# Performance work log

Hardware: AMD Instinct MI355X
Metric: run time of the kernel (lower is better)

## Reference

```python
import jax, jax.numpy as jnp
import numpy as np

B, A, C = 16, 16384, 81
TOP_K = 50
CONF_THRESH = 0.5
IOU_THRESH = 0.5
VAR0, VAR1 = 0.1, 0.2          # cfg['variance']
IMG_HW = 1.0                   # cfg['min_dim']/img_size = 320/320
MIN_SIZE = 0.0
NEG = -jnp.inf


def setup_inputs() -> dict:
    key = jax.random.key(0)
    k1, k2, k3 = jax.random.split(key, 3)
    conf_preds = jax.random.uniform(k1, (B, A, C), dtype=jnp.float32)
    loc_delta = jax.random.normal(k2, (B, A, 4), dtype=jnp.float32)
    anchors = jax.random.uniform(k3, (A, 4), dtype=jnp.float32)  # cxcywh priors in [0,1)
    return {"conf_preds": conf_preds, "loc_delta": loc_delta, "anchors": anchors}


def _decode_clip(loc, anchors):
    # SSD decode: cxcy = prior_cxcy + loc_xy*v0*prior_wh ; wh = prior_wh*exp(loc_wh*v1)
    cxcy = anchors[..., :2] + loc[..., :2] * VAR0 * anchors[..., 2:]
    wh = anchors[..., 2:] * jnp.exp(loc[..., 2:] * VAR1)
    x1y1 = cxcy - wh * 0.5
    x2y2 = x1y1 + wh
    boxes = jnp.concatenate([x1y1, x2y2], axis=-1)  # [..., 4] xyxy
    return jnp.clip(boxes, 0.0, IMG_HW)            # clip_boxes_to_image((1,1))


def _nms_single(boxes, s):
    # boxes: [A,4] xyxy, s: [A] scores with invalid entries already at -inf.
    # Greedy NMS, fixed TOP_K iterations (torchvision semantics: suppress iou > thresh).
    areas = (boxes[:, 2] - boxes[:, 0]) * (boxes[:, 3] - boxes[:, 1])

    def step(s, _):
        i = jnp.argmax(s)
        take = s[i] > NEG
        b = boxes[i]
        xx1 = jnp.maximum(b[0], boxes[:, 0])
        yy1 = jnp.maximum(b[1], boxes[:, 1])
        xx2 = jnp.minimum(b[2], boxes[:, 2])
        yy2 = jnp.minimum(b[3], boxes[:, 3])
        inter = jnp.maximum(xx2 - xx1, 0.0) * jnp.maximum(yy2 - yy1, 0.0)
        iou = inter / (areas[i] + areas - inter)
        s = jnp.where(take & (iou > IOU_THRESH), NEG, s)
        s = s.at[i].set(NEG)  # guarantee progress
        return s, (i, take)

    _, (idx, take) = jax.lax.scan(step, s, None, length=TOP_K)
    return idx, take  # [TOP_K] int, [TOP_K] bool


def reference(conf_preds, loc_delta, anchors):
    boxes = _decode_clip(loc_delta, anchors)                # [B,A,4]
    conf = jnp.transpose(conf_preds, (0, 2, 1))             # [B,C,A]
    # remove_small_boxes(min_size=0) as a mask (all-true here, kept for fidelity)
    w = boxes[..., 2] - boxes[..., 0]
    h = boxes[..., 3] - boxes[..., 1]
    valid = (w >= MIN_SIZE) & (h >= MIN_SIZE)               # [B,A]
    masked = jnp.where((conf > CONF_THRESH) & valid[:, None, :], conf, NEG)  # [B,C,A]

    sg = jax.lax.stop_gradient
    nms_c = jax.vmap(_nms_single, in_axes=(None, 0))        # over classes
    nms_bc = jax.vmap(nms_c, in_axes=(0, 0))                # over batch
    idx, take = nms_bc(sg(boxes), sg(masked))               # [B,C,K]

    scores_sel = jnp.take_along_axis(conf, idx, axis=2)     # [B,C,K]
    b_idx = jnp.arange(boxes.shape[0])[:, None, None]
    boxes_sel = boxes[b_idx, idx]                           # [B,C,K,4]
    preds = jnp.concatenate([
        jnp.where(take, scores_sel, 0.0)[..., None],
        jnp.where(take[..., None], boxes_sel, 0.0),
    ], axis=-1)                                             # [B,C,K,5]
    return preds
```

## Files before the change

### kernel.cpp

```cpp
#include <hip/hip_runtime.h>
#include <math.h>

#define NB 16
#define NA 16384
#define NC 81
#define TOPK 50
#define TRC 4096
#define NEGF (-__builtin_inff())
#define SUPC 0.5000000298023223876953125

typedef unsigned long long ull;

#define WS_CONFT_OFF  ((size_t)4194304)
#define WS_FULL  (WS_CONFT_OFF + (size_t)NB * NC * NA * 2)

__global__ __launch_bounds__(256) void decode_k(const float* __restrict__ loc,
                                                const float* __restrict__ anc,
                                                float* __restrict__ boxes) {
#pragma clang fp contract(off)
    int i = blockIdx.x * 256 + threadIdx.x;
    if (i >= NB * NA) return;
    int a = i & (NA - 1);
    float4 an = ((const float4*)anc)[a];
    float4 ld = ((const float4*)loc)[i];
    float cx = an.x + (ld.x * 0.1f) * an.z;
    float cy = an.y + (ld.y * 0.1f) * an.w;
    float w = an.z * (float)exp((double)(ld.z * 0.2f));
    float h = an.w * (float)exp((double)(ld.w * 0.2f));
    float x1 = cx - w * 0.5f;
    float y1 = cy - h * 0.5f;
    float x2 = x1 + w;
    float y2 = y1 + h;
    x1 = fminf(fmaxf(x1, 0.f), 1.f);
    y1 = fminf(fmaxf(y1, 0.f), 1.f);
    x2 = fminf(fmaxf(x2, 0.f), 1.f);
    y2 = fminf(fmaxf(y2, 0.f), 1.f);
    ((float4*)boxes)[i] = make_float4(x1, y1, x2, y2);
}

__device__ __forceinline__ unsigned short enc_code(float v) {
    unsigned short e = 0xFFFFu;
    if (v > 0.5f) e = (unsigned short)(511u - ((__float_as_uint(v) >> 14) & 0x1FFu));
    return e;
}

#define TSLAB 256
__global__ __launch_bounds__(256) void transq_k(const float* __restrict__ conf,
                                                unsigned short* __restrict__ confT) {
    __shared__ unsigned short code[TSLAB * NC];
    const int b = blockIdx.y;
    const int slab = blockIdx.x;
    const float4* src = (const float4*)(conf + ((size_t)b * NA + (size_t)slab * TSLAB) * NC);
    const int t = threadIdx.x;
    for (int i = t; i < (TSLAB * NC) / 4; i += 256) {
        float4 v = src[i];
        unsigned f = 4u * (unsigned)i;
        unsigned a = f / (unsigned)NC;
        unsigned c = f - a * (unsigned)NC;
        code[c * TSLAB + a] = enc_code(v.x);
        if (++c == NC) { c = 0; ++a; }
        code[c * TSLAB + a] = enc_code(v.y);
        if (++c == NC) { c = 0; ++a; }
        code[c * TSLAB + a] = enc_code(v.z);
        if (++c == NC) { c = 0; ++a; }
        code[c * TSLAB + a] = enc_code(v.w);
    }
    __syncthreads();
    const int lane = t & 63, wv = t >> 6;
    for (int c = wv; c < NC; c += 4) {
        ull v = *(const ull*)&code[c * TSLAB + lane * 4];
        *(ull*)(confT + ((size_t)b * NC + c) * NA + (size_t)slab * TSLAB + lane * 4) = v;
    }
}

__global__ __launch_bounds__(256, 8) void nmsB4_k(const unsigned short* __restrict__ confT,
                                                  const float* __restrict__ conf,
                                                  const float* __restrict__ boxes,
                                                  float* __restrict__ out) {
#pragma clang fp contract(off)
    const int blk = blockIdx.x;
    const int b = blk / NC, c = blk - b * NC;
    const int t = threadIdx.x;
    const int lane = t & 63, wv = t >> 6;

    __shared__ unsigned short s_ix[TRC];
    __shared__ unsigned s_off[513];
    __shared__ unsigned s_aux[512];
    __shared__ float s_acc[TOPK][5];
    __shared__ float4 s_cbox[256];
    __shared__ unsigned long long s_kill[4];
    __shared__ int s_ctrl[16];

    const uint4* row8 = (const uint4*)(confT + ((size_t)b * NC + c) * NA);
    const float* cp = conf + ((size_t)b * NA) * NC + c;
    const float4* bb = (const float4*)boxes + (size_t)b * NA;
    float* orow = out + ((size_t)b * NC + c) * (TOPK * 5);

    for (int i = t; i < 512; i += 256) s_aux[i] = 0u;
    if (t == 0) { s_ctrl[0] = 0; s_ctrl[8] = 0; s_ctrl[12] = 0; }
    __syncthreads();
#pragma unroll
    for (int r = 0; r < 8; ++r) {
        uint4 q = row8[t + 256 * r];
        unsigned w;
        w = q.x; if ((w & 0xFFFFu) != 0xFFFFu) atomicAdd(&s_aux[w & 0xFFFFu], 1u);
                 if ((w >> 16)     != 0xFFFFu) atomicAdd(&s_aux[w >> 16], 1u);
        w = q.y; if ((w & 0xFFFFu) != 0xFFFFu) atomicAdd(&s_aux[w & 0xFFFFu], 1u);
                 if ((w >> 16)     != 0xFFFFu) atomicAdd(&s_aux[w >> 16], 1u);
        w = q.z; if ((w & 0xFFFFu) != 0xFFFFu) atomicAdd(&s_aux[w & 0xFFFFu], 1u);
                 if ((w >> 16)     != 0xFFFFu) atomicAdd(&s_aux[w >> 16], 1u);
        w = q.w; if ((w & 0xFFFFu) != 0xFFFFu) atomicAdd(&s_aux[w & 0xFFFFu], 1u);
                 if ((w >> 16)     != 0xFFFFu) atomicAdd(&s_aux[w >> 16], 1u);
    }
    __syncthreads();
    for (int i = t; i < 512; i += 256) atomicMax(&s_ctrl[8], (int)s_aux[i]);
    if (t == 0) s_off[0] = 0u;
    for (int i = t; i < 512; i += 256) s_off[i + 1] = s_aux[i];
    __syncthreads();
    for (int d = 1; d < 512; d <<= 1) {
        int i0 = 1 + t, i1 = 257 + t;
        unsigned v0 = (i0 - d >= 1) ? s_off[i0 - d] : 0u;
        unsigned v1 = (i1 - d >= 1) ? s_off[i1 - d] : 0u;
        __syncthreads();
        s_off[i0] += v0;
        s_off[i1] += v1;
        __syncthreads();
    }

    if (s_ctrl[8] <= TRC) {
        while (true) {
            if (t == 0) {
                int lo = s_ctrl[12];
                int hi = lo;
                while (hi < 512 && s_off[hi + 1] - s_off[lo] <= (unsigned)TRC) hi++;
                s_ctrl[13] = hi;
            }
            __syncthreads();
            const int trLo = s_ctrl[12], trHi = s_ctrl[13];
            const unsigned tbase = s_off[trLo], tend = s_off[trHi];
            if (tbase == tend) break;
            for (int i = trLo + t; i < trHi; i += 256) s_aux[i] = s_off[i] - tbase;
            __syncthreads();
#pragma unroll
            for (int r = 0; r < 8; ++r) {
                uint4 q = row8[t + 256 * r];
                int a0i = 8 * (t + 256 * r);
                unsigned w; int bk;
                w = q.x;
                bk = (int)(w & 0xFFFFu); if (bk >= trLo && bk < trHi) s_ix[atomicAdd(&s_aux[bk], 1u)] = (unsigned short)(a0i + 0);
                bk = (int)(w >> 16);     if (bk >= trLo && bk < trHi) s_ix[atomicAdd(&s_aux[bk], 1u)] = (unsigned short)(a0i + 1);
                w = q.y;
                bk = (int)(w & 0xFFFFu); if (bk >= trLo && bk < trHi) s_ix[atomicAdd(&s_aux[bk], 1u)] = (unsigned short)(a0i + 2);
                bk = (int)(w >> 16);     if (bk >= trLo && bk < trHi) s_ix[atomicAdd(&s_aux[bk], 1u)] = (unsigned short)(a0i + 3);
                w = q.z;
                bk = (int)(w & 0xFFFFu); if (bk >= trLo && bk < trHi) s_ix[atomicAdd(&s_aux[bk], 1u)] = (unsigned short)(a0i + 4);
                bk = (int)(w >> 16);     if (bk >= trLo && bk < trHi) s_ix[atomicAdd(&s_aux[bk], 1u)] = (unsigned short)(a0i + 5);
                w = q.w;
                bk = (int)(w & 0xFFFFu); if (bk >= trLo && bk < trHi) s_ix[atomicAdd(&s_aux[bk], 1u)] = (unsigned short)(a0i + 6);
                bk = (int)(w >> 16);     if (bk >= trLo && bk < trHi) s_ix[atomicAdd(&s_aux[bk], 1u)] = (unsigned short)(a0i + 7);
            }
            if (t == 0) s_ctrl[7] = trLo;
            __syncthreads();

            while (true) {
                if (t == 0) {
                    int bp = s_ctrl[7];
                    int mode;
                    if (bp >= trHi || s_off[bp] >= tend) {
                        mode = 2;
                    } else {
                        unsigned pos = s_off[bp] - tbase;
                        int bpl = bp;
                        unsigned q = pos;
                        for (int w = 0; w < 4; ++w) {
                            s_ctrl[2 + w] = (int)q;
                            while (bpl < trHi && (s_off[bpl + 1] - tbase - q) <= 64u) bpl++;
                            q = (bpl < trHi) ? s_off[bpl] - tbase : tend - tbase;
                        }
                        s_ctrl[6] = (int)q;
                        s_ctrl[7] = bpl;
                        mode = 0;
                        if (q == pos) {
                            mode = 1;
                            s_ctrl[9] = (int)pos;
                            s_ctrl[10] = (int)(s_off[bp + 1] - tbase);
                            s_ctrl[7] = bp + 1;
                        }
                    }
                    s_ctrl[11] = mode;
                }
                __syncthreads();
                const int mode = s_ctrl[11];
                if (mode == 2) break;
                const int nacc0 = s_ctrl[0];

                if (mode == 0) {
                    const unsigned q0 = (unsigned)s_ctrl[2 + wv];
                    const unsigned q1 = (unsigned)s_ctrl[3 + wv];
                    const int mw = (int)(q1 - q0);
                    const bool valid = lane < mw;
                    int ii = (int)q0 + lane; if (ii > TRC - 1) ii = TRC - 1;
                    int a = valid ? (int)s_ix[ii] : 0;
                    float4 bxv = bb[a];
                    if (!valid) bxv = make_float4(0.f, 0.f, 0.f, 0.f);
                    s_cbox[wv * 64 + lane] = bxv;
                    float mar = (bxv.z - bxv.x) * (bxv.w - bxv.y);
                    bool kill = !valid;
                    for (int j = 0; j < nacc0; ++j) {
                        float xx1 = fmaxf(s_acc[j][0], bxv.x), yy1 = fmaxf(s_acc[j][1], bxv.y);
                        float xx2 = fminf(s_acc[j][2], bxv.z), yy2 = fminf(s_acc[j][3], bxv.w);
                        float iw = fmaxf(xx2 - xx1, 0.f), ih = fmaxf(yy2 - yy1, 0.f);
                        float inter = iw * ih;
                        float den = (s_acc[j][4] + mar) - inter;
                        if ((double)inter > (double)den * SUPC) kill = true;
                    }
                    unsigned long long km = __ballot(kill);
                    if (lane == 0) s_kill[wv] = km;
                    __syncthreads();

                    if (wv == 0) {
                        int na = nacc0;
                        for (int cc = 0; cc < 4 && na < TOPK; ++cc) {
                            const unsigned e0 = (unsigned)s_ctrl[2 + cc];
                            const unsigned e1 = (unsigned)s_ctrl[3 + cc];
                            const int mc = (int)(e1 - e0);
                            if (mc <= 0) continue;
                            unsigned long long alive = ~s_kill[cc];
                            if (mc < 64) alive &= (1ull << mc) - 1ull;
                            int jj = (int)e0 + lane; if (jj > TRC - 1) jj = TRC - 1;
                            int aj = (lane < mc) ? (int)s_ix[jj] : 0;
                            float myscore = cp[(size_t)aj * NC];
                            float4 mybx = s_cbox[cc * 64 + lane];
                            float mar2 = (mybx.z - mybx.x) * (mybx.w - mybx.y);
                            for (int j = nacc0; j < na && alive; ++j) {
                                float xx1 = fmaxf(s_acc[j][0], mybx.x), yy1 = fmaxf(s_acc[j][1], mybx.y);
                                float xx2 = fminf(s_acc[j][2], mybx.z), yy2 = fminf(s_acc[j][3], mybx.w);
                                float iw = fmaxf(xx2 - xx1, 0.f), ih = fmaxf(yy2 - yy1, 0.f);
                                float inter = iw * ih;
                                float den = (s_acc[j][4] + mar2) - inter;
                                bool sup = ((double)inter > (double)den * SUPC);
                                alive &= ~__ballot(sup);
                            }
                            unsigned long long mykey =
                                ((unsigned long long)__float_as_uint(myscore) << 32) |
                                (unsigned)(16383 - aj);
                            while (alive && na < TOPK) {
                                unsigned long long kk = ((alive >> lane) & 1ull) ? mykey : 0ull;
                                int src = lane;
                                for (int off = 32; off; off >>= 1) {
                                    unsigned long long ok = __shfl_xor(kk, off);
                                    int osrc = __shfl_xor(src, off);
                                    if (ok > kk) { kk = ok; src = osrc; }
                                }
                                float4 wb = s_cbox[cc * 64 + src];
                                float wscore = __shfl(myscore, src);
                                float war = (wb.z - wb.x) * (wb.w - wb.y);
                                if (lane == 0) {
                                    orow[na * 5 + 0] = wscore;
                                    orow[na * 5 + 1] = wb.x; orow[na * 5 + 2] = wb.y;
                                    orow[na * 5 + 3] = wb.z; orow[na * 5 + 4] = wb.w;
                                    s_acc[na][0] = wb.x; s_acc[na][1] = wb.y;
                                    s_acc[na][2] = wb.z; s_acc[na][3] = wb.w;
                                    s_acc[na][4] = war;
                                }
                                na++;
                                alive &= ~(1ull << src);
                                if (alive) {
                                    float xx1 = fmaxf(wb.x, mybx.x), yy1 = fmaxf(wb.y, mybx.y);
                                    float xx2 = fminf(wb.z, mybx.z), yy2 = fminf(wb.w, mybx.w);
                                    float iw = fmaxf(xx2 - xx1, 0.f), ih = fmaxf(yy2 - yy1, 0.f);
                                    float inter = iw * ih;
                                    float den = (war + mar2) - inter;
                                    bool sup = ((double)inter > (double)den * SUPC);
                                    alive &= ~__ballot(sup);
                                }
                            }
                        }
                        if (lane == 0) s_ctrl[0] = na;
                    }
                    __syncthreads();
                } else {
                    const int e0 = s_ctrl[9], e1 = s_ctrl[10];
                    if (wv == 0) {
                        int na = s_ctrl[0];
                        while (na < TOPK) {
                            unsigned long long bk = 0ull; int bpos = 0;
                            for (int i = e0 + lane; i < e1; i += 64) {
                                int av = (int)s_ix[i];
                                if (av != 0xFFFF) {
                                    float v = cp[(size_t)av * NC];
                                    unsigned long long k =
                                        ((unsigned long long)__float_as_uint(v) << 32) |
                                        (unsigned)(16383 - av);
                                    if (k > bk) { bk = k; bpos = i; }
                                }
                            }
                            for (int off = 32; off; off >>= 1) {
                                unsigned long long ok = __shfl_xor(bk, off);
                                int op = __shfl_xor(bpos, off);
                                if (ok > bk) { bk = ok; bpos = op; }
                            }
                            if (bk == 0ull) break;
                            int a = (int)s_ix[bpos];
                            float wscore = __uint_as_float((unsigned)(bk >> 32));
                            if (lane == 0) s_ix[bpos] = 0xFFFFu;
                            float4 wb = bb[a];
                            float war = (wb.z - wb.x) * (wb.w - wb.y);
                            bool sup = false;
                            if (lane < na) {
                                float xx1 = fmaxf(s_acc[lane][0], wb.x), yy1 = fmaxf(s_acc[lane][1], wb.y);
                                float xx2 = fminf(s_acc[lane][2], wb.z), yy2 = fminf(s_acc[lane][3], wb.w);
                                float iw = fmaxf(xx2 - xx1, 0.f), ih = fmaxf(yy2 - yy1, 0.f);
                                float inter = iw * ih;
                                float den = (s_acc[lane][4] + war) - inter;
                                sup = ((double)inter > (double)den * SUPC);
                            }
                            if (__ballot(sup) == 0ull) {
                                if (lane == 0) {
                                    orow[na * 5 + 0] = wscore;
                                    orow[na * 5 + 1] = wb.x; orow[na * 5 + 2] = wb.y;
                                    orow[na * 5 + 3] = wb.z; orow[na * 5 + 4] = wb.w;
                                    s_acc[na][0] = wb.x; s_acc[na][1] = wb.y;
                                    s_acc[na][2] = wb.z; s_acc[na][3] = wb.w;
                                    s_acc[na][4] = war;
                                }
                                na++;
                            }
                        }
                        if (lane == 0) s_ctrl[0] = na;
                    }
                    __syncthreads();
                }
                if (s_ctrl[0] >= TOPK) break;
            }
            if (s_ctrl[0] >= TOPK || trHi >= 512) break;
            if (t == 0) s_ctrl[12] = trHi;
            __syncthreads();
        }
    } else {
        float hi = 1.0f, delta = 0.02f;
        while (true) {
            if (s_ctrl[0] >= TOPK || hi <= 0.5f) break;
            float lo = fmaxf(hi - delta, 0.5f);
            if (t == 0) s_ctrl[1] = 0;
            __syncthreads();
            for (int a = t; a < NA; a += 256) {
                float v = cp[(size_t)a * NC];
                if (v > lo && v <= hi) {
                    int p = atomicAdd(&s_ctrl[1], 1);
                    if (p < TRC) s_ix[p] = (unsigned short)a;
                }
            }
            __syncthreads();
            int m = s_ctrl[1];
            if (m > TRC) { delta *= 0.5f; continue; }
            if (wv == 0) {
                int na = s_ctrl[0];
                while (na < TOPK) {
                    unsigned long long bk = 0ull; int bpos = 0;
                    for (int i = lane; i < m; i += 64) {
                        int av = (int)s_ix[i];
                        if (av != 0xFFFF) {
                            float v = cp[(size_t)av * NC];
                            unsigned long long k =
                                ((unsigned long long)__float_as_uint(v) << 32) |
                                (unsigned)(16383 - av);
                            if (k > bk) { bk = k; bpos = i; }
                        }
                    }
                    for (int off = 32; off; off >>= 1) {
                        unsigned long long ok = __shfl_xor(bk, off);
                        int op = __shfl_xor(bpos, off);
                        if (ok > bk) { bk = ok; bpos = op; }
                    }
                    if (bk == 0ull) break;
                    int a = (int)s_ix[bpos];
                    float wscore = __uint_as_float((unsigned)(bk >> 32));
                    if (lane == 0) s_ix[bpos] = 0xFFFFu;
                    float4 wb = bb[a];
                    float war = (wb.z - wb.x) * (wb.w - wb.y);
                    bool sup = false;
                    if (lane < na) {
                        float xx1 = fmaxf(s_acc[lane][0], wb.x), yy1 = fmaxf(s_acc[lane][1], wb.y);
                        float xx2 = fminf(s_acc[lane][2], wb.z), yy2 = fminf(s_acc[lane][3], wb.w);
                        float iw = fmaxf(xx2 - xx1, 0.f), ih = fmaxf(yy2 - yy1, 0.f);
                        float inter = iw * ih;
                        float den = (s_acc[lane][4] + war) - inter;
                        sup = ((double)inter > (double)den * SUPC);
                    }
                    if (__ballot(sup) == 0ull) {
                        if (lane == 0) {
                            orow[na * 5 + 0] = wscore;
                            orow[na * 5 + 1] = wb.x; orow[na * 5 + 2] = wb.y;
                            orow[na * 5 + 3] = wb.z; orow[na * 5 + 4] = wb.w;
                            s_acc[na][0] = wb.x; s_acc[na][1] = wb.y;
                            s_acc[na][2] = wb.z; s_acc[na][3] = wb.w;
                            s_acc[na][4] = war;
                        }
                        na++;
                    }
                }
                if (lane == 0) s_ctrl[0] = na;
            }
            __syncthreads();
            hi = lo;
        }
    }

    __syncthreads();
    const int naF = s_ctrl[0];
    for (int z = naF * 5 + t; z < TOPK * 5; z += 256) orow[z] = 0.f;
}

#define OTHREADS 1024
#define OCAP 10240
#define OJMAX 10

__global__ __launch_bounds__(OTHREADS) void nms_old_k(const float* __restrict__ conf,
                                                      const float* __restrict__ boxes,
                                                      float* __restrict__ out) {
#pragma clang fp contract(off)
    const int blk = blockIdx.x;
    const int b = blk / NC, c = blk - b * NC;
    const int t = threadIdx.x;
    const int lane = t & 63, wid = t >> 6;
    __shared__ float s_val[OCAP];
    __shared__ unsigned short s_idx[OCAP];
    __shared__ float s_ps[2][16];
    __shared__ int s_pa[2][16];
    __shared__ int s_n;
    if (t == 0) s_n = 0;
    __syncthreads();
    const float* cp = conf + ((size_t)b * NA) * NC + c;
    float v[NA / OTHREADS];
#pragma unroll
    for (int r = 0; r < NA / OTHREADS; ++r)
        v[r] = cp[(size_t)(r * OTHREADS + t) * NC];
#pragma unroll
    for (int r = 0; r < NA / OTHREADS; ++r) {
        int a = r * OTHREADS + t;
        bool alive = v[r] > 0.5f;
        unsigned long long m = __ballot(alive);
        int cnt = __popcll(m);
        int base = 0;
        if (lane == 0 && cnt) base = atomicAdd(&s_n, cnt);
        base = __shfl(base, 0);
        if (alive) {
            int p = base + __popcll(m & ((1ull << lane) - 1));
            if (p < OCAP) { s_val[p] = v[r]; s_idx[p] = (unsigned short)a; }
        }
    }
    __syncthreads();
    int n = s_n; if (n > OCAP) n = OCAP;
    const int jn = (n + OTHREADS - 1) / OTHREADS;
    const float4* bb = (const float4*)boxes + (size_t)b * NA;
    float sc[OJMAX]; float4 bx[OJMAX]; int ia[OJMAX];
#pragma unroll
    for (int j = 0; j < OJMAX; ++j) {
        sc[j] = NEGF; ia[j] = 0x7fffffff; bx[j] = make_float4(0.f, 0.f, 0.f, 0.f);
        int p = j * OTHREADS + t;
        if (p < n) { sc[j] = s_val[p]; ia[j] = (int)s_idx[p]; bx[j] = bb[ia[j]]; }
    }
    float* orow = out + (size_t)blk * (TOPK * 5);
    int k = 0;
    for (; k < TOPK; ++k) {
        float ms = NEGF; int ma = 0x7fffffff;
#pragma unroll
        for (int j = 0; j < OJMAX; ++j) {
            if (j < jn) {
                bool better = (sc[j] > ms) || (sc[j] == ms && ia[j] < ma);
                ms = better ? sc[j] : ms;
                ma = better ? ia[j] : ma;
            }
        }
#pragma unroll
        for (int off = 32; off; off >>= 1) {
            float os = __shfl_xor(ms, off);
            int oa = __shfl_xor(ma, off);
            if (os > ms || (os == ms && oa < ma)) { ms = os; ma = oa; }
        }
        int pb = k & 1;
        if (lane == 0) { s_ps[pb][wid] = ms; s_pa[pb][wid] = ma; }
        __syncthreads();
        float wsv = NEGF; int wa = 0x7fffffff;
#pragma unroll
        for (int w = 0; w < 16; ++w) {
            float os = s_ps[pb][w]; int oa = s_pa[pb][w];
            if (os > wsv || (os == wsv && oa < wa)) { wsv = os; wa = oa; }
        }
        if (!(wsv > NEGF)) break;
        float4 wb = bb[wa];
        float warea = (wb.z - wb.x) * (wb.w - wb.y);
        if (t == 0) {
            orow[k * 5 + 0] = wsv;
            orow[k * 5 + 1] = wb.x; orow[k * 5 + 2] = wb.y;
            orow[k * 5 + 3] = wb.z; orow[k * 5 + 4] = wb.w;
        }
#pragma unroll
        for (int j = 0; j < OJMAX; ++j) {
            if (j < jn) {
                float xx1 = fmaxf(wb.x, bx[j].x);
                float yy1 = fmaxf(wb.y, bx[j].y);
                float xx2 = fminf(wb.z, bx[j].z);
                float yy2 = fminf(wb.w, bx[j].w);
                float iw = fmaxf(xx2 - xx1, 0.f);
                float ih = fmaxf(yy2 - yy1, 0.f);
                float inter = iw * ih;
                float aj = (bx[j].z - bx[j].x) * (bx[j].w - bx[j].y);
                float denom = (warea + aj) - inter;
                bool supp = ((double)inter > (double)denom * SUPC) || (ia[j] == wa);
                if (supp) sc[j] = NEGF;
            }
        }
    }
    for (int z = k * 5 + t; z < TOPK * 5; z += OTHREADS) orow[z] = 0.f;
}

extern "C" void kernel_launch(void* const* d_in, const int* in_sizes, int n_in,
                              void* d_out, int out_size, void* d_ws, size_t ws_size,
                              hipStream_t stream) {
    const float* conf = (const float*)d_in[0];
    const float* loc  = (const float*)d_in[1];
    const float* anc  = (const float*)d_in[2];
    float* boxes = (float*)d_ws;

    decode_k<<<(NB * NA + 255) / 256, 256, 0, stream>>>(loc, anc, boxes);

    if (ws_size >= WS_FULL) {
        unsigned short* confT = (unsigned short*)((char*)d_ws + WS_CONFT_OFF);
        dim3 tg(NA / TSLAB, NB);
        transq_k<<<tg, 256, 0, stream>>>(conf, confT);
        nmsB4_k<<<NB * NC, 256, 0, stream>>>(confT, conf, boxes, (float*)d_out);
    } else {
        nms_old_k<<<NB * NC, OTHREADS, 0, stream>>>(conf, boxes, (float*)d_out);
    }
}
```

Baseline: 231.1 us.

## Quantize transposed confidence codes to 8-bit buckets and enlarge candidate tile

The transposed score codes shrink from 16-bit codes over 512 buckets to 8-bit codes over 255 buckets, halving confT write and read traffic. The transpose now packs bytes row-major into shared memory and gathers them per class on readout. The histogram and scatter loops handle 16 anchors per uint4. The candidate buffer TRC grows to 8960 to fit the coarser buckets, and occupancy hints drop from 8 to 6 blocks. Coarser buckets mean larger candidate groups per bucket for the NMS stage, and the bigger shared buffer lowers occupancy.

```diff
diff --git a/kernel.cpp b/kernel.cpp
--- a/kernel.cpp
+++ b/kernel.cpp
@@ -5,14 +5,15 @@
 #define NA 16384
 #define NC 81
 #define TOPK 50
-#define TRC 4096
+#define NBK 255
+#define TRC 8960
 #define NEGF (-__builtin_inff())
 #define SUPC 0.5000000298023223876953125
 
 typedef unsigned long long ull;
 
 #define WS_CONFT_OFF  ((size_t)4194304)
-#define WS_FULL  (WS_CONFT_OFF + (size_t)NB * NC * NA * 2)
+#define WS_FULL  (WS_CONFT_OFF + (size_t)NB * NC * NA)
 
 __global__ __launch_bounds__(256) void decode_k(const float* __restrict__ loc,
                                                 const float* __restrict__ anc,
@@ -38,42 +39,40 @@
     ((float4*)boxes)[i] = make_float4(x1, y1, x2, y2);
 }
 
-__device__ __forceinline__ unsigned short enc_code(float v) {
-    unsigned short e = 0xFFFFu;
-    if (v > 0.5f) e = (unsigned short)(511u - ((__float_as_uint(v) >> 14) & 0x1FFu));
+__device__ __forceinline__ unsigned enc8(float v) {
+    unsigned e = 0xFFu;
+    if (v > 0.5f) {
+        unsigned d = 255u - ((__float_as_uint(v) >> 15) & 0xFFu);
+        e = (d > 254u) ? 254u : d;
+    }
     return e;
 }
 
-#define TSLAB 256
+#define TSLAB 512
 __global__ __launch_bounds__(256) void transq_k(const float* __restrict__ conf,
-                                                unsigned short* __restrict__ confT) {
-    __shared__ unsigned short code[TSLAB * NC];
+                                                unsigned char* __restrict__ confT) {
+    __shared__ unsigned char code[TSLAB * NC];
     const int b = blockIdx.y;
     const int slab = blockIdx.x;
     const float4* src = (const float4*)(conf + ((size_t)b * NA + (size_t)slab * TSLAB) * NC);
     const int t = threadIdx.x;
     for (int i = t; i < (TSLAB * NC) / 4; i += 256) {
         float4 v = src[i];
-        unsigned f = 4u * (unsigned)i;
-        unsigned a = f / (unsigned)NC;
-        unsigned c = f - a * (unsigned)NC;
-        code[c * TSLAB + a] = enc_code(v.x);
-        if (++c == NC) { c = 0; ++a; }
-        code[c * TSLAB + a] = enc_code(v.y);
-        if (++c == NC) { c = 0; ++a; }
-        code[c * TSLAB + a] = enc_code(v.z);
-        if (++c == NC) { c = 0; ++a; }
-        code[c * TSLAB + a] = enc_code(v.w);
+        unsigned wrd = enc8(v.x) | (enc8(v.y) << 8) | (enc8(v.z) << 16) | (enc8(v.w) << 24);
+        *(unsigned*)&code[4 * i] = wrd;
     }
     __syncthreads();
     const int lane = t & 63, wv = t >> 6;
     for (int c = wv; c < NC; c += 4) {
-        ull v = *(const ull*)&code[c * TSLAB + lane * 4];
-        *(ull*)(confT + ((size_t)b * NC + c) * NA + (size_t)slab * TSLAB + lane * 4) = v;
+        ull v = 0ull;
+#pragma unroll
+        for (int j = 0; j < 8; ++j)
+            v |= (ull)code[(8 * lane + j) * NC + c] << (8 * j);
+        *(ull*)(confT + ((size_t)b * NC + c) * NA + (size_t)slab * TSLAB + 8 * lane) = v;
     }
 }
 
-__global__ __launch_bounds__(256, 8) void nmsB4_k(const unsigned short* __restrict__ confT,
+__global__ __launch_bounds__(256, 6) void nmsB5_k(const unsigned char* __restrict__ confT,
                                                   const float* __restrict__ conf,
                                                   const float* __restrict__ boxes,
                                                   float* __restrict__ out) {
@@ -84,46 +83,43 @@
     const int lane = t & 63, wv = t >> 6;
 
     __shared__ unsigned short s_ix[TRC];
-    __shared__ unsigned s_off[513];
-    __shared__ unsigned s_aux[512];
+    __shared__ unsigned s_off[NBK + 1];
+    __shared__ unsigned s_aux[NBK];
     __shared__ float s_acc[TOPK][5];
     __shared__ float4 s_cbox[256];
     __shared__ unsigned long long s_kill[4];
     __shared__ int s_ctrl[16];
 
-    const uint4* row8 = (const uint4*)(confT + ((size_t)b * NC + c) * NA);
+    const uint4* row16 = (const uint4*)(confT + ((size_t)b * NC + c) * NA);
     const float* cp = conf + ((size_t)b * NA) * NC + c;
     const float4* bb = (const float4*)boxes + (size_t)b * NA;
     float* orow = out + ((size_t)b * NC + c) * (TOPK * 5);
 
-    for (int i = t; i < 512; i += 256) s_aux[i] = 0u;
+    if (t < NBK) s_aux[t] = 0u;
     if (t == 0) { s_ctrl[0] = 0; s_ctrl[8] = 0; s_ctrl[12] = 0; }
     __syncthreads();
 #pragma unroll
-    for (int r = 0; r < 8; ++r) {
-        uint4 q = row8[t + 256 * r];
-        unsigned w;
-        w = q.x; if ((w & 0xFFFFu) != 0xFFFFu) atomicAdd(&s_aux[w & 0xFFFFu], 1u);
-                 if ((w >> 16)     != 0xFFFFu) atomicAdd(&s_aux[w >> 16], 1u);
-        w = q.y; if ((w & 0xFFFFu) != 0xFFFFu) atomicAdd(&s_aux[w & 0xFFFFu], 1u);
-                 if ((w >> 16)     != 0xFFFFu) atomicAdd(&s_aux[w >> 16], 1u);
-        w = q.z; if ((w & 0xFFFFu) != 0xFFFFu) atomicAdd(&s_aux[w & 0xFFFFu], 1u);
-                 if ((w >> 16)     != 0xFFFFu) atomicAdd(&s_aux[w >> 16], 1u);
-        w = q.w; if ((w & 0xFFFFu) != 0xFFFFu) atomicAdd(&s_aux[w & 0xFFFFu], 1u);
-                 if ((w >> 16)     != 0xFFFFu) atomicAdd(&s_aux[w >> 16], 1u);
-    }
-    __syncthreads();
-    for (int i = t; i < 512; i += 256) atomicMax(&s_ctrl[8], (int)s_aux[i]);
+    for (int r = 0; r < 4; ++r) {
+        uint4 q = row16[t + 256 * r];
+        unsigned wrds[4] = {q.x, q.y, q.z, q.w};
+#pragma unroll
+        for (int m = 0; m < 4; ++m)
+#pragma unroll
+            for (int k = 0; k < 4; ++k) {
+                unsigned bk = (wrds[m] >> (8 * k)) & 0xFFu;
+                if (bk != 0xFFu) atomicAdd(&s_aux[bk], 1u);
+            }
+    }
+    __syncthreads();
+    if (t < NBK) atomicMax(&s_ctrl[8], (int)s_aux[t]);
     if (t == 0) s_off[0] = 0u;
-    for (int i = t; i < 512; i += 256) s_off[i + 1] = s_aux[i];
-    __syncthreads();
-    for (int d = 1; d < 512; d <<= 1) {
-        int i0 = 1 + t, i1 = 257 + t;
-        unsigned v0 = (i0 - d >= 1) ? s_off[i0 - d] : 0u;
-        unsigned v1 = (i1 - d >= 1) ? s_off[i1 - d] : 0u;
+    if (t < NBK) s_off[t + 1] = s_aux[t];
+    __syncthreads();
+    for (int d = 1; d < 256; d <<= 1) {
+        unsigned v0 = 0u;
+        if (t < NBK) v0 = (1 + t - d >= 1) ? s_off[1 + t - d] : 0u;
         __syncthreads();
-        s_off[i0] += v0;
-        s_off[i1] += v1;
+        if (t < NBK) s_off[1 + t] += v0;
         __syncthreads();
     }
 
@@ -132,7 +128,7 @@
             if (t == 0) {
                 int lo = s_ctrl[12];
                 int hi = lo;
-                while (hi < 512 && s_off[hi + 1] - s_off[lo] <= (unsigned)TRC) hi++;
+                while (hi < NBK && s_off[hi + 1] - s_off[lo] <= (unsigned)TRC) hi++;
                 s_ctrl[13] = hi;
             }
             __syncthreads();
@@ -142,22 +138,19 @@
             for (int i = trLo + t; i < trHi; i += 256) s_aux[i] = s_off[i] - tbase;
             __syncthreads();
 #pragma unroll
-            for (int r = 0; r < 8; ++r) {
-                uint4 q = row8[t + 256 * r];
-                int a0i = 8 * (t + 256 * r);
-                unsigned w; int bk;
-                w = q.x;
-                bk = (int)(w & 0xFFFFu); if (bk >= trLo && bk < trHi) s_ix[atomicAdd(&s_aux[bk], 1u)] = (unsigned short)(a0i + 0);
-                bk = (int)(w >> 16);     if (bk >= trLo && bk < trHi) s_ix[atomicAdd(&s_aux[bk], 1u)] = (unsigned short)(a0i + 1);
-                w = q.y;
-                bk = (int)(w & 0xFFFFu); if (bk >= trLo && bk < trHi) s_ix[atomicAdd(&s_aux[bk], 1u)] = (unsigned short)(a0i + 2);
-                bk = (int)(w >> 16);     if (bk >= trLo && bk < trHi) s_ix[atomicAdd(&s_aux[bk], 1u)] = (unsigned short)(a0i + 3);
-                w = q.z;
-                bk = (int)(w & 0xFFFFu); if (bk >= trLo && bk < trHi) s_ix[atomicAdd(&s_aux[bk], 1u)] = (unsigned short)(a0i + 4);
-                bk = (int)(w >> 16);     if (bk >= trLo && bk < trHi) s_ix[atomicAdd(&s_aux[bk], 1u)] = (unsigned short)(a0i + 5);
-                w = q.w;
-                bk = (int)(w & 0xFFFFu); if (bk >= trLo && bk < trHi) s_ix[atomicAdd(&s_aux[bk], 1u)] = (unsigned short)(a0i + 6);
-                bk = (int)(w >> 16);     if (bk >= trLo && bk < trHi) s_ix[atomicAdd(&s_aux[bk], 1u)] = (unsigned short)(a0i + 7);
+            for (int r = 0; r < 4; ++r) {
+                uint4 q = row16[t + 256 * r];
+                unsigned wrds[4] = {q.x, q.y, q.z, q.w};
+                int base_a = 16 * (t + 256 * r);
+#pragma unroll
+                for (int m = 0; m < 4; ++m)
+#pragma unroll
+                    for (int k = 0; k < 4; ++k) {
+                        int bk = (int)((wrds[m] >> (8 * k)) & 0xFFu);
+                        if (bk >= trLo && bk < trHi)
+                            s_ix[atomicAdd(&s_aux[bk], 1u)] =
+                                (unsigned short)(base_a + 4 * m + k);
+                    }
             }
             if (t == 0) s_ctrl[7] = trLo;
             __syncthreads();
@@ -333,7 +326,7 @@
                 }
                 if (s_ctrl[0] >= TOPK) break;
             }
-            if (s_ctrl[0] >= TOPK || trHi >= 512) break;
+            if (s_ctrl[0] >= TOPK || trHi >= NBK) break;
             if (t == 0) s_ctrl[12] = trHi;
             __syncthreads();
         }
@@ -527,10 +520,10 @@
     decode_k<<<(NB * NA + 255) / 256, 256, 0, stream>>>(loc, anc, boxes);
 
     if (ws_size >= WS_FULL) {
-        unsigned short* confT = (unsigned short*)((char*)d_ws + WS_CONFT_OFF);
+        unsigned char* confT = (unsigned char*)((char*)d_ws + WS_CONFT_OFF);
         dim3 tg(NA / TSLAB, NB);
         transq_k<<<tg, 256, 0, stream>>>(conf, confT);
-        nmsB4_k<<<NB * NC, 256, 0, stream>>>(confT, conf, boxes, (float*)d_out);
+        nmsB5_k<<<NB * NC, 256, 0, stream>>>(confT, conf, boxes, (float*)d_out);
     } else {
         nms_old_k<<<NB * NC, OTHREADS, 0, stream>>>(conf, boxes, (float*)d_out);
     }
```

Result: faster. 210.6 us (-8.9%).
